# Optimization experiments

Hardware: AMD Instinct MI355X
Metric: run time of the kernel (lower is better)

## Reference

```python
import jax, jax.numpy as jnp
import numpy as np


def _normalized_adj(A):
    # get_a: d = 0.5*I, a = off-diagonal ones + A, a2 = d @ a @ d
    off = jnp.array([[0., 1., 1.], [1., 0., 1.], [1., 1., 0.]], dtype=A.dtype)
    a = off + A
    d = 0.5 * jnp.eye(3, dtype=A.dtype)
    return d @ a @ d  # [3,3]


def setup_inputs() -> dict:
    key = jax.random.key(0)
    k1, k2 = jax.random.split(key)
    B = 8192
    x = jax.random.normal(k1, (B, 3, 10), dtype=jnp.float32)
    A = jnp.eye(3, dtype=jnp.float32)  # get_A() returns identity; Parameter init
    stdv = 1.0 / np.sqrt(10.0)
    W = jax.random.uniform(k2, (10, 10), dtype=jnp.float32, minval=-stdv, maxval=stdv)
    return {"x": x, "A": A, "W": W}


def reference(x, A, W):
    # adjacency is detached in the torch forward
    adj = jax.lax.stop_gradient(_normalized_adj(A))  # [3,3], shared across batch
    # GraphConvolution: adj @ (x @ W)
    support = jnp.einsum('bnf,fo->bno', x, W)          # [B,3,10]
    h = jnp.einsum('nm,bmo->bno', adj, support)        # [B,3,10]
    # permute -> [B,10,3]; AvgPool1d(2) on length 3 -> length 1: mean of nodes 0,1
    pooled = 0.5 * (h[:, 0, :] + h[:, 1, :])           # [B,10]
    # ScaleDotProductAttention over the batch axis
    score = jax.nn.softmax(pooled @ pooled.T, axis=-1)  # [B,B]
    v = score @ pooled                                  # [B,10]
    return v
```

## Files before the change

kernel.cpp:

```cpp
#include <hip/hip_runtime.h>
#include <math.h>

#define BROWS 8192
#define F 10
#define TJ 512
#define QPITCH 20
#define APITCH (TJ + 8)
#define LOG2E 1.44269504088896340736f

#if __has_builtin(__builtin_amdgcn_exp2f)
#define EXP2F(x) __builtin_amdgcn_exp2f(x)
#else
#define EXP2F(x) exp2f(x)
#endif

typedef _Float16 half4 __attribute__((ext_vector_type(4)));
typedef __fp16 fp16x2 __attribute__((ext_vector_type(2)));
typedef float floatx4 __attribute__((ext_vector_type(4)));

__device__ __forceinline__ half4 exp4_to_h4(float a, float b, float c, float d) {
#if __has_builtin(__builtin_amdgcn_cvt_pkrtz)
    union { fp16x2 h2[2]; half4 h4; } u;
    u.h2[0] = __builtin_amdgcn_cvt_pkrtz(EXP2F(a), EXP2F(b));
    u.h2[1] = __builtin_amdgcn_cvt_pkrtz(EXP2F(c), EXP2F(d));
    return u.h4;
#else
    half4 r;
    r[0] = (_Float16)EXP2F(a); r[1] = (_Float16)EXP2F(b);
    r[2] = (_Float16)EXP2F(c); r[3] = (_Float16)EXP2F(d);
    return r;
#endif
}

__device__ __forceinline__ uint32_t pack2(_Float16 a, _Float16 b) {
    union { _Float16 h[2]; uint32_t u; } x;
    x.h[0] = a; x.h[1] = b;
    return x.u;
}

__global__ void pooled_kernel(const float* __restrict__ x,
                              const float* __restrict__ A,
                              const float* __restrict__ W,
                              float* __restrict__ pooled) {
    int b = blockIdx.x * blockDim.x + threadIdx.x;
    if (b >= BROWS) return;

    float c0 = 0.125f * (1.0f + A[0] + A[3]);
    float c1 = 0.125f * (1.0f + A[1] + A[4]);
    float c2 = 0.125f * (2.0f + A[2] + A[5]);

    const float2* xb = (const float2*)(x + (size_t)b * 3 * F);
    float xv[3 * F];
#pragma unroll
    for (int k = 0; k < 15; ++k) {
        float2 t = xb[k];
        xv[2 * k] = t.x; xv[2 * k + 1] = t.y;
    }

    float y[F];
#pragma unroll
    for (int f = 0; f < F; ++f)
        y[f] = c0 * xv[f] + c1 * xv[F + f] + c2 * xv[2 * F + f];

#pragma unroll
    for (int o = 0; o < F; ++o) {
        float acc = 0.0f;
#pragma unroll
        for (int f = 0; f < F; ++f)
            acc = fmaf(y[f], W[f * F + o], acc);
        pooled[(size_t)b * F + o] = acc;
    }
}

__global__ void attn_kernel(const float* __restrict__ pooled,
                            float* __restrict__ out) {
    __shared__ __align__(16) _Float16 qrow[TJ * QPITCH];
    __shared__ __align__(16) _Float16 augT[16 * APITCH];
    __shared__ __align__(16) float red[8 * 16 * 12];

    const int tid  = threadIdx.x;
    const int wave = tid >> 6;
    const int lane = tid & 63;
    const int m    = lane & 15;
    const int quad = lane >> 4;
    const int irow = blockIdx.x * 16 + m;

    half4 b1;
#pragma unroll
    for (int idx = 0; idx < 4; ++idx) {
        int f = quad * 4 + idx;
        float v = (f < F) ? pooled[(size_t)irow * F + f] * LOG2E : 0.0f;
        b1[idx] = (_Float16)v;
    }

    for (int e = tid; e < 6 * APITCH; e += 512) {
        int n = 10 + e / APITCH;
        int j = e % APITCH;
        augT[n * APITCH + j] = (n == 10) ? (_Float16)1.0f : (_Float16)0.0f;
    }

    floatx4 acc0 = {0.f, 0.f, 0.f, 0.f};
    floatx4 acc1 = {0.f, 0.f, 0.f, 0.f};

    float2 s0, s1, s2, s3, s4;
    {
        const float2* src = (const float2*)(pooled + (size_t)tid * F);
        s0 = src[0]; s1 = src[1]; s2 = src[2]; s3 = src[3]; s4 = src[4];
    }

    for (int t = 0; t < BROWS / TJ; ++t) {
        __syncthreads();
        {
            _Float16 h0 = (_Float16)s0.x, h1 = (_Float16)s0.y;
            _Float16 h2 = (_Float16)s1.x, h3 = (_Float16)s1.y;
            _Float16 h4 = (_Float16)s2.x, h5 = (_Float16)s2.y;
            _Float16 h6 = (_Float16)s3.x, h7 = (_Float16)s3.y;
            _Float16 h8 = (_Float16)s4.x, h9 = (_Float16)s4.y;

            uint32_t* qr = (uint32_t*)&qrow[tid * QPITCH];
            qr[0] = pack2(h0, h1); qr[1] = pack2(h2, h3); qr[2] = pack2(h4, h5);
            qr[3] = pack2(h6, h7); qr[4] = pack2(h8, h9);
            qr[5] = 0u; qr[6] = 0u; qr[7] = 0u;

            augT[0 * APITCH + tid] = h0; augT[1 * APITCH + tid] = h1;
            augT[2 * APITCH + tid] = h2; augT[3 * APITCH + tid] = h3;
            augT[4 * APITCH + tid] = h4; augT[5 * APITCH + tid] = h5;
            augT[6 * APITCH + tid] = h6; augT[7 * APITCH + tid] = h7;
            augT[8 * APITCH + tid] = h8; augT[9 * APITCH + tid] = h9;
        }
        __syncthreads();

        if (t + 1 < BROWS / TJ) {
            const float2* src = (const float2*)(pooled +
                                (size_t)((t + 1) * TJ + tid) * F);
            s0 = src[0]; s1 = src[1]; s2 = src[2]; s3 = src[3]; s4 = src[4];
        }

#pragma unroll
        for (int c = 0; c < 4; ++c) {
            const int jb = wave * 64 + c * 16;
            half4 a1 = *(const half4*)&qrow[(jb + m) * QPITCH + quad * 4];
            floatx4 d1 = __builtin_amdgcn_mfma_f32_16x16x16f16(
                a1, b1, (floatx4){0.f, 0.f, 0.f, 0.f}, 0, 0, 0);
            half4 a2 = exp4_to_h4(d1[0], d1[1], d1[2], d1[3]);
            half4 ag = *(const half4*)&augT[m * APITCH + jb + quad * 4];
            if (c & 1)
                acc1 = __builtin_amdgcn_mfma_f32_16x16x16f16(ag, a2, acc1, 0, 0, 0);
            else
                acc0 = __builtin_amdgcn_mfma_f32_16x16x16f16(ag, a2, acc0, 0, 0, 0);
        }
    }

    floatx4 acc = acc0 + acc1;

    if (quad < 3)
        *(floatx4*)&red[(wave * 16 + m) * 12 + quad * 4] = acc;
    __syncthreads();

    if (tid < 160) {
        const int i16 = tid / 10;
        const int f   = tid % 10;
        float sum = 0.0f, l = 0.0f;
#pragma unroll
        for (int w = 0; w < 8; ++w) {
            sum += red[(w * 16 + i16) * 12 + f];
            l   += red[(w * 16 + i16) * 12 + 10];
        }
        out[(size_t)(blockIdx.x * 16 + i16) * F + f] = sum / l;
    }
}

extern "C" void kernel_launch(void* const* d_in, const int* in_sizes, int n_in,
                              void* d_out, int out_size, void* d_ws, size_t ws_size,
                              hipStream_t stream) {
    const float* x = (const float*)d_in[0];
    const float* A = (const float*)d_in[1];
    const float* W = (const float*)d_in[2];
    float* out = (float*)d_out;
    float* pooled = (float*)d_ws;

    pooled_kernel<<<BROWS / 64, 64, 0, stream>>>(x, A, W, pooled);
    attn_kernel<<<BROWS / 16, 512, 0, stream>>>(pooled, out);
}
```

Measured before the change: 77.98 us.

## Precompute fp16 padded and transposed pooled layouts and DMA tiles into LDS

After: 76.46 us. No clear change (-2.0%).

```diff
diff --git a/kernel.cpp b/kernel.cpp
--- a/kernel.cpp
+++ b/kernel.cpp
@@ -4,8 +4,9 @@
 #define BROWS 8192
 #define F 10
 #define TJ 512
-#define QPITCH 20
-#define APITCH (TJ + 8)
+#define QP 20
+#define AP 520
+#define NT (BROWS / TJ)
 #define LOG2E 1.44269504088896340736f
 
 #if __has_builtin(__builtin_amdgcn_exp2f)
@@ -38,10 +39,21 @@
     return x.u;
 }
 
+__device__ __forceinline__ void gload_lds16(const void* g, void* l) {
+#if __has_builtin(__builtin_amdgcn_global_load_lds)
+    __builtin_amdgcn_global_load_lds(
+        (const __attribute__((address_space(1))) void*)g,
+        (__attribute__((address_space(3))) void*)l, 16, 0, 0);
+#else
+    *(float4*)l = *(const float4*)g;
+#endif
+}
+
 __global__ void pooled_kernel(const float* __restrict__ x,
                               const float* __restrict__ A,
                               const float* __restrict__ W,
-                              float* __restrict__ pooled) {
+                              _Float16* __restrict__ poolQ,
+                              _Float16* __restrict__ poolT) {
     int b = blockIdx.x * blockDim.x + threadIdx.x;
     if (b >= BROWS) return;
 
@@ -62,20 +74,35 @@
     for (int f = 0; f < F; ++f)
         y[f] = c0 * xv[f] + c1 * xv[F + f] + c2 * xv[2 * F + f];
 
+    float po[F];
 #pragma unroll
     for (int o = 0; o < F; ++o) {
         float acc = 0.0f;
 #pragma unroll
         for (int f = 0; f < F; ++f)
             acc = fmaf(y[f], W[f * F + o], acc);
-        pooled[(size_t)b * F + o] = acc;
-    }
-}
-
-__global__ void attn_kernel(const float* __restrict__ pooled,
+        po[o] = acc;
+    }
+
+    uint2* qd = (uint2*)(poolQ + (size_t)b * QP);
+    qd[0] = make_uint2(pack2((_Float16)po[0], (_Float16)po[1]),
+                       pack2((_Float16)po[2], (_Float16)po[3]));
+    qd[1] = make_uint2(pack2((_Float16)po[4], (_Float16)po[5]),
+                       pack2((_Float16)po[6], (_Float16)po[7]));
+    qd[2] = make_uint2(pack2((_Float16)po[8], (_Float16)po[9]), 0u);
+    qd[3] = make_uint2(0u, 0u);
+    qd[4] = make_uint2(0u, 0u);
+
+#pragma unroll
+    for (int o = 0; o < F; ++o)
+        poolT[(size_t)o * BROWS + b] = (_Float16)po[o];
+}
+
+__global__ void attn_kernel(const _Float16* __restrict__ poolQ,
+                            const _Float16* __restrict__ poolT,
                             float* __restrict__ out) {
-    __shared__ __align__(16) _Float16 qrow[TJ * QPITCH];
-    __shared__ __align__(16) _Float16 augT[16 * APITCH];
+    __shared__ __align__(16) _Float16 qbuf[2][TJ * QP];
+    __shared__ __align__(16) _Float16 abuf[2][16 * AP];
     __shared__ __align__(16) float red[8 * 16 * 12];
 
     const int tid  = threadIdx.x;
@@ -89,66 +116,53 @@
 #pragma unroll
     for (int idx = 0; idx < 4; ++idx) {
         int f = quad * 4 + idx;
-        float v = (f < F) ? pooled[(size_t)irow * F + f] * LOG2E : 0.0f;
+        float v = (f < F) ? (float)poolQ[(size_t)irow * QP + f] * LOG2E : 0.0f;
         b1[idx] = (_Float16)v;
     }
 
-    for (int e = tid; e < 6 * APITCH; e += 512) {
-        int n = 10 + e / APITCH;
-        int j = e % APITCH;
-        augT[n * APITCH + j] = (n == 10) ? (_Float16)1.0f : (_Float16)0.0f;
-    }
+    for (int e = tid; e < 2 * 6 * AP; e += 512) {
+        int bufi = e / (6 * AP);
+        int r    = e % (6 * AP);
+        int n    = 10 + r / AP;
+        int j    = r % AP;
+        abuf[bufi][n * AP + j] = (n == 10) ? (_Float16)1.0f : (_Float16)0.0f;
+    }
+
+    auto dma_tile = [&](int t, int bufi) {
+        const char* qs = (const char*)poolQ + (size_t)t * TJ * QP * 2;
+        char* qd = (char*)&qbuf[bufi][0];
+        for (int d = wave; d < 20; d += 8)
+            gload_lds16(qs + d * 1024 + lane * 16, qd + d * 1024 + lane * 16);
+        char* ad = (char*)&abuf[bufi][0];
+        for (int n = wave; n < F; n += 8)
+            gload_lds16((const char*)(poolT + (size_t)n * BROWS + t * TJ) + lane * 16,
+                        ad + n * (AP * 2) + lane * 16);
+    };
 
     floatx4 acc0 = {0.f, 0.f, 0.f, 0.f};
     floatx4 acc1 = {0.f, 0.f, 0.f, 0.f};
 
-    float2 s0, s1, s2, s3, s4;
-    {
-        const float2* src = (const float2*)(pooled + (size_t)tid * F);
-        s0 = src[0]; s1 = src[1]; s2 = src[2]; s3 = src[3]; s4 = src[4];
-    }
-
-    for (int t = 0; t < BROWS / TJ; ++t) {
-        __syncthreads();
-        {
-            _Float16 h0 = (_Float16)s0.x, h1 = (_Float16)s0.y;
-            _Float16 h2 = (_Float16)s1.x, h3 = (_Float16)s1.y;
-            _Float16 h4 = (_Float16)s2.x, h5 = (_Float16)s2.y;
-            _Float16 h6 = (_Float16)s3.x, h7 = (_Float16)s3.y;
-            _Float16 h8 = (_Float16)s4.x, h9 = (_Float16)s4.y;
-
-            uint32_t* qr = (uint32_t*)&qrow[tid * QPITCH];
-            qr[0] = pack2(h0, h1); qr[1] = pack2(h2, h3); qr[2] = pack2(h4, h5);
-            qr[3] = pack2(h6, h7); qr[4] = pack2(h8, h9);
-            qr[5] = 0u; qr[6] = 0u; qr[7] = 0u;
-
-            augT[0 * APITCH + tid] = h0; augT[1 * APITCH + tid] = h1;
-            augT[2 * APITCH + tid] = h2; augT[3 * APITCH + tid] = h3;
-            augT[4 * APITCH + tid] = h4; augT[5 * APITCH + tid] = h5;
-            augT[6 * APITCH + tid] = h6; augT[7 * APITCH + tid] = h7;
-            augT[8 * APITCH + tid] = h8; augT[9 * APITCH + tid] = h9;
-        }
-        __syncthreads();
-
-        if (t + 1 < BROWS / TJ) {
-            const float2* src = (const float2*)(pooled +
-                                (size_t)((t + 1) * TJ + tid) * F);
-            s0 = src[0]; s1 = src[1]; s2 = src[2]; s3 = src[3]; s4 = src[4];
-        }
+    dma_tile(0, 0);
+    __syncthreads();
+
+    for (int t = 0; t < NT; ++t) {
+        const int buf = t & 1;
+        if (t + 1 < NT) dma_tile(t + 1, buf ^ 1);
 
 #pragma unroll
         for (int c = 0; c < 4; ++c) {
             const int jb = wave * 64 + c * 16;
-            half4 a1 = *(const half4*)&qrow[(jb + m) * QPITCH + quad * 4];
+            half4 a1 = *(const half4*)&qbuf[buf][(jb + m) * QP + quad * 4];
             floatx4 d1 = __builtin_amdgcn_mfma_f32_16x16x16f16(
                 a1, b1, (floatx4){0.f, 0.f, 0.f, 0.f}, 0, 0, 0);
             half4 a2 = exp4_to_h4(d1[0], d1[1], d1[2], d1[3]);
-            half4 ag = *(const half4*)&augT[m * APITCH + jb + quad * 4];
+            half4 ag = *(const half4*)&abuf[buf][m * AP + jb + quad * 4];
             if (c & 1)
                 acc1 = __builtin_amdgcn_mfma_f32_16x16x16f16(ag, a2, acc1, 0, 0, 0);
             else
                 acc0 = __builtin_amdgcn_mfma_f32_16x16x16f16(ag, a2, acc0, 0, 0, 0);
         }
+        __syncthreads();
     }
 
     floatx4 acc = acc0 + acc1;
@@ -177,8 +191,10 @@
     const float* A = (const float*)d_in[1];
     const float* W = (const float*)d_in[2];
     float* out = (float*)d_out;
-    float* pooled = (float*)d_ws;
-
-    pooled_kernel<<<BROWS / 64, 64, 0, stream>>>(x, A, W, pooled);
-    attn_kernel<<<BROWS / 16, 512, 0, stream>>>(pooled, out);
-}
+
+    _Float16* poolQ = (_Float16*)d_ws;
+    _Float16* poolT = (_Float16*)((char*)d_ws + 327680);
+
+    pooled_kernel<<<BROWS / 64, 64, 0, stream>>>(x, A, W, poolQ, poolT);
+    attn_kernel<<<BROWS / 16, 512, 0, stream>>>(poolQ, poolT, out);
+}
```
